# Optimization experiments

Measured on AMD Instinct MI355X. Metric: run time of the kernel, lower is better.

## Reference

```python
import jax, jax.numpy as jnp
import numpy as np

PATCH = 7
STRIDE = 1


def extract_patches(im, p=PATCH, stride=STRIDE):
    # im: [b, c, h, w] -> patches [b, N, c*p*p] (torch.nn.Unfold-style layout)
    pt = jax.lax.conv_general_dilated_patches(
        im, filter_shape=(p, p), window_strides=(stride, stride), padding='VALID')
    # pt: [b, c*p*p, h', w']
    b, d = pt.shape[0], pt.shape[1]
    return pt.reshape(b, d, -1).transpose(0, 2, 1)  # [b, N, d]


def coherence_swd(xp, yp, rand):
    # xp, yp: [N, d]; rand: [d, P]
    r = rand / jnp.std(rand, axis=0, keepdims=True, ddof=1)  # torch.std is unbiased
    px = xp @ r  # [N, P]
    py = yp @ r  # [N, P]
    ix = jnp.argsort(px, axis=0).T  # [P, N]
    iy = jnp.argsort(py, axis=0).T  # [P, N]
    # Gather full patch vectors by per-projection sorted order, L1 distance.
    # xp[ix]: [P, N, d] -- the big irregular-gather intermediate.
    diff = jnp.abs(xp[ix] - yp[iy])  # [P, N, d]
    # loss = (1/P) * sum_p mean(|...|_p); each term has identical size -> plain mean
    return diff.mean()


def setup_inputs() -> dict:
    key = jax.random.key(0)
    k1, k2, k3 = jax.random.split(key, 3)
    b, c, h, w = 1, 3, 96, 96
    d = c * PATCH * PATCH  # 147
    num_proj = 256
    x = jax.random.normal(k1, (b, c, h, w), dtype=jnp.float32)
    y = jax.random.normal(k2, (b, c, h, w), dtype=jnp.float32)
    rand = jax.random.normal(k3, (d, num_proj), dtype=jnp.float32)
    return {"x": x, "y": y, "rand": rand}


def reference(x, y, rand):
    x_patches = extract_patches(x)  # [b, N, d]
    y_patches = extract_patches(y)
    losses = jax.vmap(coherence_swd, in_axes=(0, 0, None))(x_patches, y_patches, rand)  # [b]
    return losses.mean()  # batch_reduction='mean'
```

## Files before the change

### kernel.cpp

```cpp
#include <hip/hip_runtime.h>

#define HH 96
#define WW 96
#define OH 90
#define OW 90
#define NPATCH 8100
#define DD 147
#define DPAD 148
#define NPROJ 256
#define TN 32
#define SORT_T 512
#define NBUCK 4096
#define KPT 16
#define PGRP 16
#define NCH 64
#define KPB2 128

typedef float vf2 __attribute__((ext_vector_type(2)));

__device__ __forceinline__ float l1_fp8x4(unsigned xw, unsigned yw, float acc) {
    const vf2 a0 = __builtin_amdgcn_cvt_pk_f32_fp8((int)xw, false);
    const vf2 a1 = __builtin_amdgcn_cvt_pk_f32_fp8((int)xw, true);
    const vf2 b0 = __builtin_amdgcn_cvt_pk_f32_fp8((int)yw, false);
    const vf2 b1 = __builtin_amdgcn_cvt_pk_f32_fp8((int)yw, true);
    acc += fabsf(a0.x - b0.x);
    acc += fabsf(a0.y - b0.y);
    acc += fabsf(a1.x - b1.x);
    acc += fabsf(a1.y - b1.y);
    return acc;
}

__global__ __launch_bounds__(512, 4)
void patch_proj_kernel(const float* __restrict__ x, const float* __restrict__ y,
                       const float* __restrict__ rnd,
                       int* __restrict__ xm8, int* __restrict__ ym8,
                       int* __restrict__ xt8, int* __restrict__ yt8,
                       float* __restrict__ pxT, float* __restrict__ pyT,
                       float* __restrict__ out)
{
    __shared__ float s[TN * DPAD];
    const int tid = threadIdx.x;
    const int n0 = blockIdx.x * TN;
    const int img = blockIdx.y;
    const float* __restrict__ src = img ? y : x;
    int* __restrict__ m8 = img ? ym8 : xm8;
    int* __restrict__ t8 = img ? yt8 : xt8;
    float* __restrict__ pT = img ? pyT : pxT;
    if (blockIdx.x == 0 && img == 0 && tid == 0) out[0] = 0.0f;

    for (int idx = tid; idx < TN * DPAD; idx += 512) {
        const int t = idx / DPAD;
        const int d = idx - t * DPAD;
        const int n = n0 + t;
        float v = 0.f;
        if (n < NPATCH && d < DD) {
            const int oy = n / OW, ox = n - oy * OW;
            const int c  = d / 49, r  = d - c * 49;
            const int di = r / 7,  dj = r - di * 7;
            v = src[c * (HH * WW) + (oy + di) * WW + (ox + dj)];
        }
        s[idx] = v;
    }
    __syncthreads();

    for (int idx = tid; idx < TN * 40; idx += 512) {
        const int t = idx / 40;
        const int u = idx - t * 40;
        const int n = n0 + t;
        if (n >= NPATCH) continue;
        int w = 0;
        if (u < 32) {
            const int d = 4 * u;
            w = __builtin_amdgcn_cvt_pk_fp8_f32(s[t*DPAD+d],   s[t*DPAD+d+1], w, false);
            w = __builtin_amdgcn_cvt_pk_fp8_f32(s[t*DPAD+d+2], s[t*DPAD+d+3], w, true);
            m8[(size_t)n * 32 + u] = w;
        } else {
            const int ut = u - 32;
            const int d = 128 + 4 * ut;
            const float v0 = (d     < DPAD) ? s[t*DPAD+d]     : 0.f;
            const float v1 = (d + 1 < DPAD) ? s[t*DPAD+d+1]   : 0.f;
            const float v2 = (d + 2 < DPAD) ? s[t*DPAD+d+2]   : 0.f;
            const float v3 = (d + 3 < DPAD) ? s[t*DPAD+d+3]   : 0.f;
            w = __builtin_amdgcn_cvt_pk_fp8_f32(v0, v1, w, false);
            w = __builtin_amdgcn_cvt_pk_fp8_f32(v2, v3, w, true);
            t8[(size_t)n * 8 + ut] = w;
        }
    }

    const int q2 = tid & 127;
    const int t0 = (tid >> 7) * 8;
    const float2* __restrict__ rnd2 = (const float2*)rnd;

    float acc[8][2];
#pragma unroll
    for (int t = 0; t < 8; ++t) { acc[t][0] = 0.f; acc[t][1] = 0.f; }

    for (int d = 0; d < 144; d += 4) {
        const float2 r0 = rnd2[(d + 0) * 128 + q2];
        const float2 r1 = rnd2[(d + 1) * 128 + q2];
        const float2 r2 = rnd2[(d + 2) * 128 + q2];
        const float2 r3 = rnd2[(d + 3) * 128 + q2];
#pragma unroll
        for (int t = 0; t < 8; ++t) {
            const float4 v = *(const float4*)&s[(t0 + t) * DPAD + d];
            acc[t][0] += v.x * r0.x + v.y * r1.x + v.z * r2.x + v.w * r3.x;
            acc[t][1] += v.x * r0.y + v.y * r1.y + v.z * r2.y + v.w * r3.y;
        }
    }
    {
        const float2 r0 = rnd2[144 * 128 + q2];
        const float2 r1 = rnd2[145 * 128 + q2];
        const float2 r2 = rnd2[146 * 128 + q2];
#pragma unroll
        for (int t = 0; t < 8; ++t) {
            const float4 v = *(const float4*)&s[(t0 + t) * DPAD + 144];
            acc[t][0] += v.x * r0.x + v.y * r1.x + v.z * r2.x;
            acc[t][1] += v.x * r0.y + v.y * r1.y + v.z * r2.y;
        }
    }

    const int nb = n0 + t0;
#pragma unroll
    for (int r = 0; r < 2; ++r) {
        float* row = pT + (size_t)(2 * q2 + r) * NPATCH + nb;
        if (nb + 7 < NPATCH) {
            float4 lo, hi;
            lo.x = acc[0][r]; lo.y = acc[1][r]; lo.z = acc[2][r]; lo.w = acc[3][r];
            hi.x = acc[4][r]; hi.y = acc[5][r]; hi.z = acc[6][r]; hi.w = acc[7][r];
            ((float4*)row)[0] = lo;
            ((float4*)row)[1] = hi;
        } else {
#pragma unroll
            for (int t = 0; t < 8; ++t)
                if (nb + t < NPATCH) row[t] = acc[t][r];
        }
    }
}

__global__ __launch_bounds__(SORT_T, 4)
void rank_kernel(const float* __restrict__ pT,
                 unsigned short* __restrict__ rxOut,
                 unsigned short* __restrict__ iyOut)
{
    __shared__ unsigned hist[NBUCK];
    __shared__ unsigned cnt[NBUCK];
    __shared__ float    skey[8192];
    __shared__ unsigned wsum[8];
    const int pb = blockIdx.x;
    const int tid = threadIdx.x;
    const int lane = tid & 63;
    const float* col = pT + (size_t)pb * NPATCH;

    {
        uint4 z = make_uint4(0, 0, 0, 0);
        ((uint4*)hist)[tid] = z;
        ((uint4*)hist)[tid + SORT_T] = z;
    }
    __syncthreads();

    float k[KPT];
    int bk[KPT];
#pragma unroll
    for (int t = 0; t < KPT; ++t) {
        const int i = tid + SORT_T * t;
        if (i < NPATCH) {
            const float v = col[i];
            k[t] = v;
            int b = (int)((v + 51.2f) * 40.0f);
            b = b < 0 ? 0 : (b > NBUCK - 1 ? NBUCK - 1 : b);
            bk[t] = b;
            atomicAdd(&hist[b], 1u);
        } else {
            k[t] = 0.f;
            bk[t] = -1;
        }
    }
    __syncthreads();

    {
        const int b0 = tid * 8;
        unsigned h[8];
#pragma unroll
        for (int q = 0; q < 8; ++q) h[q] = hist[b0 + q];
        unsigned tsum = 0;
#pragma unroll
        for (int q = 0; q < 8; ++q) tsum += h[q];
        unsigned acc = tsum;
#pragma unroll
        for (int d = 1; d < 64; d <<= 1) {
            const unsigned v = __shfl_up(acc, d, 64);
            if (lane >= d) acc += v;
        }
        const unsigned wexcl = acc - tsum;
        if (lane == 63) wsum[tid >> 6] = acc;
        __syncthreads();
        if (tid == 0) {
            unsigned roff = 0;
#pragma unroll
            for (int w = 0; w < 8; ++w) {
                const unsigned tt = wsum[w];
                wsum[w] = roff;
                roff += tt;
            }
        }
        __syncthreads();
        unsigned run = wsum[tid >> 6] + wexcl;
#pragma unroll
        for (int q = 0; q < 8; ++q) { cnt[b0 + q] = run; run += h[q]; }
    }
    __syncthreads();

#pragma unroll
    for (int t = 0; t < KPT; ++t) {
        if (bk[t] >= 0) {
            const unsigned pos = atomicAdd(&cnt[bk[t]], 1u);
            skey[pos] = k[t];
        }
    }
    __syncthreads();

#pragma unroll
    for (int t = 0; t < KPT; ++t) {
        const int i = tid + SORT_T * t;
        if (bk[t] < 0) continue;
        const int b = bk[t];
        const unsigned end = cnt[b];
        const unsigned cb = hist[b];
        const unsigned start = end - cb;
        const float myk = k[t];
        unsigned r = start;
        for (unsigned s2 = start; s2 < end; ++s2)
            r += (skey[s2] < myk) ? 1u : 0u;
        if (pb < NPROJ)
            rxOut[(size_t)pb * NPATCH + i] = (unsigned short)r;
        else
            iyOut[(size_t)(pb - NPROJ) * NPATCH + r] = (unsigned short)i;
    }
}

__global__ __launch_bounds__(256, 4)
void reduce_kernel(const uint4* __restrict__ xm8, const uint4* __restrict__ ym8,
                   const uint4* __restrict__ xt8, const uint4* __restrict__ yt8,
                   const unsigned short* __restrict__ rx,
                   const unsigned short* __restrict__ iy,
                   float* __restrict__ out)
{
    __shared__ unsigned short sp[PGRP * KPB2];
    const int p0 = blockIdx.y * PGRP;
    const int i0 = blockIdx.x * KPB2;
    const int iend = min(i0 + KPB2, NPATCH);
    const int tid = threadIdx.x;
    const int wave = tid >> 6, lane = tid & 63;

    for (int idx = tid; idx < PGRP * KPB2; idx += 256) {
        const int pp = idx >> 7, r = idx & 127;
        int src = i0 + r;
        src = src < NPATCH ? src : NPATCH - 1;
        const int p = p0 + pp;
        const unsigned short rk = rx[(size_t)p * NPATCH + src];
        const unsigned short j = iy[(size_t)p * NPATCH + rk];
        sp[idx] = j < NPATCH ? j : (unsigned short)(NPATCH - 1);
    }
    __syncthreads();

    float facc = 0.f;

    {
        const int g = lane >> 3;
        const int u = lane & 7;
#pragma unroll
        for (int it = 0; it < 4; ++it) {
            const int i = i0 + wave * 8 + it * 32;
            const uint4 xa = xm8[(size_t)i * 8 + lane];
            int jj[PGRP];
#pragma unroll
            for (int pp = 0; pp < PGRP; ++pp)
                jj[pp] = sp[pp * KPB2 + (i - i0) + g];
            uint4 ya[PGRP];
#pragma unroll
            for (int pp = 0; pp < PGRP; ++pp)
                ya[pp] = ym8[(size_t)jj[pp] * 8 + u];
            float tacc = 0.f;
#pragma unroll
            for (int pp = 0; pp < PGRP; ++pp) {
                tacc = l1_fp8x4(xa.x, ya[pp].x, tacc);
                tacc = l1_fp8x4(xa.y, ya[pp].y, tacc);
                tacc = l1_fp8x4(xa.z, ya[pp].z, tacc);
                tacc = l1_fp8x4(xa.w, ya[pp].w, tacc);
            }
            facc += (i + g < iend) ? tacc : 0.f;
        }
    }

    {
        const int g2 = lane >> 1;
        const int u2 = lane & 1;
        const int i2 = i0 + wave * 32;
        const uint4 xa = xt8[(size_t)i2 * 2 + lane];
        int jj[PGRP];
#pragma unroll
        for (int pp = 0; pp < PGRP; ++pp)
            jj[pp] = sp[pp * KPB2 + (i2 - i0) + g2];
        uint4 ya[PGRP];
#pragma unroll
        for (int pp = 0; pp < PGRP; ++pp)
            ya[pp] = yt8[(size_t)jj[pp] * 2 + u2];
        float tacc = 0.f;
#pragma unroll
        for (int pp = 0; pp < PGRP; ++pp) {
            tacc = l1_fp8x4(xa.x, ya[pp].x, tacc);
            tacc = l1_fp8x4(xa.y, ya[pp].y, tacc);
            tacc = l1_fp8x4(xa.z, ya[pp].z, tacc);
            tacc = l1_fp8x4(xa.w, ya[pp].w, tacc);
        }
        facc += (i2 + g2 < iend) ? tacc : 0.f;
    }

#pragma unroll
    for (int o = 32; o > 0; o >>= 1) facc += __shfl_down(facc, o, 64);

    __shared__ float sred[4];
    if (lane == 0) sred[wave] = facc;
    __syncthreads();
    if (tid == 0) {
        const float s = sred[0] + sred[1] + sred[2] + sred[3];
        atomicAdd(out, s * (1.0f / ((float)NPROJ * (float)NPATCH * (float)DD)));
    }
}

extern "C" void kernel_launch(void* const* d_in, const int* in_sizes, int n_in,
                              void* d_out, int out_size, void* d_ws, size_t ws_size,
                              hipStream_t stream)
{
    const float* x   = (const float*)d_in[0];
    const float* y   = (const float*)d_in[1];
    const float* rnd = (const float*)d_in[2];

    char* ws = (char*)d_ws;
    int* xm8 = (int*)(ws + 0);
    int* ym8 = (int*)(ws + 1036800);
    int* xt8 = (int*)(ws + 2073600);
    int* yt8 = (int*)(ws + 2332800);
    float* pxT = (float*)(ws + 2592000);
    float* pyT = (float*)(ws + 10886400);
    unsigned short* rx = (unsigned short*)(ws + 19180800);
    unsigned short* iy = (unsigned short*)(ws + 23328000);
    float* out = (float*)d_out;

    hipLaunchKernelGGL(patch_proj_kernel, dim3((NPATCH + TN - 1) / TN, 2), dim3(512), 0, stream,
                       x, y, rnd, xm8, ym8, xt8, yt8, pxT, pyT, out);
    hipLaunchKernelGGL(rank_kernel, dim3(2 * NPROJ), dim3(SORT_T), 0, stream,
                       pxT, rx, iy);
    hipLaunchKernelGGL(reduce_kernel, dim3(NCH, NPROJ / PGRP), dim3(256), 0, stream,
                       (const uint4*)xm8, (const uint4*)ym8,
                       (const uint4*)xt8, (const uint4*)yt8, rx, iy, out);
}
```

Before: 145.3 us.

## Compute patch projections with split-bf16 MFMA and hoist fp8 decode in reduce

Replaces the scalar FP32 patch-times-projection GEMM with bf16 MFMA 16x16x32. Each operand is split into hi/lo bf16 parts and three MFMAs are accumulated per tile to keep near-fp32 accuracy. A new prep kernel transposes and splits the random matrix, tile size doubles to 64 patches, and shared memory holds a fragment-ordered layout. In the reduce kernel, the x-side fp8 values are decoded once per row instead of per projection. The risks are an extra kernel launch and small precision differences that could change sort ranks.

Result: faster. 133.1 us (-8.4%).

```diff
diff --git a/kernel.cpp b/kernel.cpp
--- a/kernel.cpp
+++ b/kernel.cpp
@@ -6,9 +6,10 @@
 #define OW 90
 #define NPATCH 8100
 #define DD 147
-#define DPAD 148
 #define NPROJ 256
-#define TN 32
+#define TN 64
+#define KPAD 160
+#define NKS 5
 #define SORT_T 512
 #define NBUCK 4096
 #define KPT 16
@@ -17,28 +18,43 @@
 #define KPB2 128
 
 typedef float vf2 __attribute__((ext_vector_type(2)));
-
-__device__ __forceinline__ float l1_fp8x4(unsigned xw, unsigned yw, float acc) {
-    const vf2 a0 = __builtin_amdgcn_cvt_pk_f32_fp8((int)xw, false);
-    const vf2 a1 = __builtin_amdgcn_cvt_pk_f32_fp8((int)xw, true);
-    const vf2 b0 = __builtin_amdgcn_cvt_pk_f32_fp8((int)yw, false);
-    const vf2 b1 = __builtin_amdgcn_cvt_pk_f32_fp8((int)yw, true);
-    acc += fabsf(a0.x - b0.x);
-    acc += fabsf(a0.y - b0.y);
-    acc += fabsf(a1.x - b1.x);
-    acc += fabsf(a1.y - b1.y);
-    return acc;
+typedef short bf16x8 __attribute__((ext_vector_type(8)));
+typedef float f32x4 __attribute__((ext_vector_type(4)));
+
+__device__ __forceinline__ unsigned short bf16_rne(float f) {
+    unsigned u = __builtin_bit_cast(unsigned, f);
+    u += 0x7FFFu + ((u >> 16) & 1u);
+    return (unsigned short)(u >> 16);
+}
+__device__ __forceinline__ float bf16_f(unsigned short h) {
+    return __builtin_bit_cast(float, (unsigned)h << 16);
+}
+
+__global__ __launch_bounds__(1024)
+void prep_rnd_kernel(const float* __restrict__ rnd,
+                     unsigned short* __restrict__ rth,
+                     unsigned short* __restrict__ rtl)
+{
+    const int idx = blockIdx.x * 1024 + threadIdx.x;
+    const int k = idx >> 8;
+    const int p = idx & 255;
+    const float v = (k < DD) ? rnd[k * NPROJ + p] : 0.f;
+    const unsigned short hi = bf16_rne(v);
+    const unsigned short lo = bf16_rne(v - bf16_f(hi));
+    rth[p * KPAD + k] = hi;
+    rtl[p * KPAD + k] = lo;
 }
 
 __global__ __launch_bounds__(512, 4)
 void patch_proj_kernel(const float* __restrict__ x, const float* __restrict__ y,
-                       const float* __restrict__ rnd,
+                       const unsigned short* __restrict__ rth,
+                       const unsigned short* __restrict__ rtl,
                        int* __restrict__ xm8, int* __restrict__ ym8,
                        int* __restrict__ xt8, int* __restrict__ yt8,
                        float* __restrict__ pxT, float* __restrict__ pyT,
                        float* __restrict__ out)
 {
-    __shared__ float s[TN * DPAD];
+    __shared__ unsigned short sh[2][TN * KPAD];
     const int tid = threadIdx.x;
     const int n0 = blockIdx.x * TN;
     const int img = blockIdx.y;
@@ -48,9 +64,9 @@
     float* __restrict__ pT = img ? pyT : pxT;
     if (blockIdx.x == 0 && img == 0 && tid == 0) out[0] = 0.0f;
 
-    for (int idx = tid; idx < TN * DPAD; idx += 512) {
-        const int t = idx / DPAD;
-        const int d = idx - t * DPAD;
+    for (int idx = tid; idx < TN * KPAD; idx += 512) {
+        const int t = idx / KPAD;
+        const int d = idx - t * KPAD;
         const int n = n0 + t;
         float v = 0.f;
         if (n < NPATCH && d < DD) {
@@ -59,7 +75,13 @@
             const int di = r / 7,  dj = r - di * 7;
             v = src[c * (HH * WW) + (oy + di) * WW + (ox + dj)];
         }
-        s[idx] = v;
+        const unsigned short hi = bf16_rne(v);
+        const unsigned short lo = bf16_rne(v - bf16_f(hi));
+        const int mt = t >> 4, r16 = t & 15;
+        const int ks = d >> 5, q = (d & 31) >> 3, j = d & 7;
+        const int fidx = (((mt * NKS + ks) * 4 + q) * 16 + r16) * 8 + j;
+        sh[0][fidx] = hi;
+        sh[1][fidx] = lo;
     }
     __syncthreads();
 
@@ -68,71 +90,65 @@
         const int u = idx - t * 40;
         const int n = n0 + t;
         if (n >= NPATCH) continue;
+        const int d = 4 * u;
+        const int mt = t >> 4, r16 = t & 15;
+        const int ks = d >> 5, q = (d & 31) >> 3, jb = d & 7;
+        const ushort4 hv = *(const ushort4*)&sh[0][(((mt * NKS + ks) * 4 + q) * 16 + r16) * 8 + jb];
         int w = 0;
-        if (u < 32) {
-            const int d = 4 * u;
-            w = __builtin_amdgcn_cvt_pk_fp8_f32(s[t*DPAD+d],   s[t*DPAD+d+1], w, false);
-            w = __builtin_amdgcn_cvt_pk_fp8_f32(s[t*DPAD+d+2], s[t*DPAD+d+3], w, true);
-            m8[(size_t)n * 32 + u] = w;
-        } else {
-            const int ut = u - 32;
-            const int d = 128 + 4 * ut;
-            const float v0 = (d     < DPAD) ? s[t*DPAD+d]     : 0.f;
-            const float v1 = (d + 1 < DPAD) ? s[t*DPAD+d+1]   : 0.f;
-            const float v2 = (d + 2 < DPAD) ? s[t*DPAD+d+2]   : 0.f;
-            const float v3 = (d + 3 < DPAD) ? s[t*DPAD+d+3]   : 0.f;
-            w = __builtin_amdgcn_cvt_pk_fp8_f32(v0, v1, w, false);
-            w = __builtin_amdgcn_cvt_pk_fp8_f32(v2, v3, w, true);
-            t8[(size_t)n * 8 + ut] = w;
-        }
-    }
-
-    const int q2 = tid & 127;
-    const int t0 = (tid >> 7) * 8;
-    const float2* __restrict__ rnd2 = (const float2*)rnd;
-
-    float acc[8][2];
-#pragma unroll
-    for (int t = 0; t < 8; ++t) { acc[t][0] = 0.f; acc[t][1] = 0.f; }
-
-    for (int d = 0; d < 144; d += 4) {
-        const float2 r0 = rnd2[(d + 0) * 128 + q2];
-        const float2 r1 = rnd2[(d + 1) * 128 + q2];
-        const float2 r2 = rnd2[(d + 2) * 128 + q2];
-        const float2 r3 = rnd2[(d + 3) * 128 + q2];
-#pragma unroll
-        for (int t = 0; t < 8; ++t) {
-            const float4 v = *(const float4*)&s[(t0 + t) * DPAD + d];
-            acc[t][0] += v.x * r0.x + v.y * r1.x + v.z * r2.x + v.w * r3.x;
-            acc[t][1] += v.x * r0.y + v.y * r1.y + v.z * r2.y + v.w * r3.y;
-        }
-    }
-    {
-        const float2 r0 = rnd2[144 * 128 + q2];
-        const float2 r1 = rnd2[145 * 128 + q2];
-        const float2 r2 = rnd2[146 * 128 + q2];
-#pragma unroll
-        for (int t = 0; t < 8; ++t) {
-            const float4 v = *(const float4*)&s[(t0 + t) * DPAD + 144];
-            acc[t][0] += v.x * r0.x + v.y * r1.x + v.z * r2.x;
-            acc[t][1] += v.x * r0.y + v.y * r1.y + v.z * r2.y;
-        }
-    }
-
-    const int nb = n0 + t0;
-#pragma unroll
-    for (int r = 0; r < 2; ++r) {
-        float* row = pT + (size_t)(2 * q2 + r) * NPATCH + nb;
-        if (nb + 7 < NPATCH) {
-            float4 lo, hi;
-            lo.x = acc[0][r]; lo.y = acc[1][r]; lo.z = acc[2][r]; lo.w = acc[3][r];
-            hi.x = acc[4][r]; hi.y = acc[5][r]; hi.z = acc[6][r]; hi.w = acc[7][r];
-            ((float4*)row)[0] = lo;
-            ((float4*)row)[1] = hi;
-        } else {
-#pragma unroll
-            for (int t = 0; t < 8; ++t)
-                if (nb + t < NPATCH) row[t] = acc[t][r];
+        w = __builtin_amdgcn_cvt_pk_fp8_f32(bf16_f(hv.x), bf16_f(hv.y), w, false);
+        w = __builtin_amdgcn_cvt_pk_fp8_f32(bf16_f(hv.z), bf16_f(hv.w), w, true);
+        if (u < 32) m8[(size_t)n * 32 + u] = w;
+        else        t8[(size_t)n * 8 + (u - 32)] = w;
+    }
+
+    const int wv = tid >> 6, lane = tid & 63;
+    const int cl = lane & 15, qk = lane >> 4;
+
+    f32x4 acc[4][2];
+#pragma unroll
+    for (int mt = 0; mt < 4; ++mt)
+#pragma unroll
+        for (int nt = 0; nt < 2; ++nt)
+            acc[mt][nt] = (f32x4){0.f, 0.f, 0.f, 0.f};
+
+#pragma unroll
+    for (int ks = 0; ks < NKS; ++ks) {
+        const int ko = ks * 32 + qk * 8;
+        bf16x8 bh[2], bl[2];
+#pragma unroll
+        for (int nt = 0; nt < 2; ++nt) {
+            const int col = wv * 32 + nt * 16 + cl;
+            bh[nt] = *(const bf16x8*)&rth[col * KPAD + ko];
+            bl[nt] = *(const bf16x8*)&rtl[col * KPAD + ko];
+        }
+#pragma unroll
+        for (int mt = 0; mt < 4; ++mt) {
+            const int base = ((mt * NKS + ks) * 64 + lane) * 8;
+            const bf16x8 ah = *(const bf16x8*)&sh[0][base];
+            const bf16x8 al = *(const bf16x8*)&sh[1][base];
+#pragma unroll
+            for (int nt = 0; nt < 2; ++nt) {
+                acc[mt][nt] = __builtin_amdgcn_mfma_f32_16x16x32_bf16(ah, bh[nt], acc[mt][nt], 0, 0, 0);
+                acc[mt][nt] = __builtin_amdgcn_mfma_f32_16x16x32_bf16(ah, bl[nt], acc[mt][nt], 0, 0, 0);
+                acc[mt][nt] = __builtin_amdgcn_mfma_f32_16x16x32_bf16(al, bh[nt], acc[mt][nt], 0, 0, 0);
+            }
+        }
+    }
+
+#pragma unroll
+    for (int mt = 0; mt < 4; ++mt) {
+        const int patch = n0 + mt * 16 + qk * 4;
+#pragma unroll
+        for (int nt = 0; nt < 2; ++nt) {
+            const int proj = wv * 32 + nt * 16 + cl;
+            float* rowp = pT + (size_t)proj * NPATCH + patch;
+            if (patch + 3 < NPATCH) {
+                *(f32x4*)rowp = acc[mt][nt];
+            } else {
+#pragma unroll
+                for (int e = 0; e < 4; ++e)
+                    if (patch + e < NPATCH) rowp[e] = acc[mt][nt][e];
+            }
         }
     }
 }
@@ -238,6 +254,28 @@
     }
 }
 
+__device__ __forceinline__ void cvt16f(const uint4 w, float* o) {
+    vf2 t;
+    t = __builtin_amdgcn_cvt_pk_f32_fp8((int)w.x, false); o[0]  = t.x; o[1]  = t.y;
+    t = __builtin_amdgcn_cvt_pk_f32_fp8((int)w.x, true);  o[2]  = t.x; o[3]  = t.y;
+    t = __builtin_amdgcn_cvt_pk_f32_fp8((int)w.y, false); o[4]  = t.x; o[5]  = t.y;
+    t = __builtin_amdgcn_cvt_pk_f32_fp8((int)w.y, true);  o[6]  = t.x; o[7]  = t.y;
+    t = __builtin_amdgcn_cvt_pk_f32_fp8((int)w.z, false); o[8]  = t.x; o[9]  = t.y;
+    t = __builtin_amdgcn_cvt_pk_f32_fp8((int)w.z, true);  o[10] = t.x; o[11] = t.y;
+    t = __builtin_amdgcn_cvt_pk_f32_fp8((int)w.w, false); o[12] = t.x; o[13] = t.y;
+    t = __builtin_amdgcn_cvt_pk_f32_fp8((int)w.w, true);  o[14] = t.x; o[15] = t.y;
+}
+
+__device__ __forceinline__ float l1_vs4(const float* xf, unsigned yw, float acc) {
+    const vf2 b0 = __builtin_amdgcn_cvt_pk_f32_fp8((int)yw, false);
+    const vf2 b1 = __builtin_amdgcn_cvt_pk_f32_fp8((int)yw, true);
+    acc += fabsf(xf[0] - b0.x);
+    acc += fabsf(xf[1] - b0.y);
+    acc += fabsf(xf[2] - b1.x);
+    acc += fabsf(xf[3] - b1.y);
+    return acc;
+}
+
 __global__ __launch_bounds__(256, 4)
 void reduce_kernel(const uint4* __restrict__ xm8, const uint4* __restrict__ ym8,
                    const uint4* __restrict__ xt8, const uint4* __restrict__ yt8,
@@ -280,13 +318,15 @@
 #pragma unroll
             for (int pp = 0; pp < PGRP; ++pp)
                 ya[pp] = ym8[(size_t)jj[pp] * 8 + u];
+            float xf[16];
+            cvt16f(xa, xf);
             float tacc = 0.f;
 #pragma unroll
             for (int pp = 0; pp < PGRP; ++pp) {
-                tacc = l1_fp8x4(xa.x, ya[pp].x, tacc);
-                tacc = l1_fp8x4(xa.y, ya[pp].y, tacc);
-                tacc = l1_fp8x4(xa.z, ya[pp].z, tacc);
-                tacc = l1_fp8x4(xa.w, ya[pp].w, tacc);
+                tacc = l1_vs4(xf + 0,  ya[pp].x, tacc);
+                tacc = l1_vs4(xf + 4,  ya[pp].y, tacc);
+                tacc = l1_vs4(xf + 8,  ya[pp].z, tacc);
+                tacc = l1_vs4(xf + 12, ya[pp].w, tacc);
             }
             facc += (i + g < iend) ? tacc : 0.f;
         }
@@ -305,13 +345,15 @@
 #pragma unroll
         for (int pp = 0; pp < PGRP; ++pp)
             ya[pp] = yt8[(size_t)jj[pp] * 2 + u2];
+        float xf[16];
+        cvt16f(xa, xf);
         float tacc = 0.f;
 #pragma unroll
         for (int pp = 0; pp < PGRP; ++pp) {
-            tacc = l1_fp8x4(xa.x, ya[pp].x, tacc);
-            tacc = l1_fp8x4(xa.y, ya[pp].y, tacc);
-            tacc = l1_fp8x4(xa.z, ya[pp].z, tacc);
-            tacc = l1_fp8x4(xa.w, ya[pp].w, tacc);
+            tacc = l1_vs4(xf + 0,  ya[pp].x, tacc);
+            tacc = l1_vs4(xf + 4,  ya[pp].y, tacc);
+            tacc = l1_vs4(xf + 8,  ya[pp].z, tacc);
+            tacc = l1_vs4(xf + 12, ya[pp].w, tacc);
         }
         facc += (i2 + g2 < iend) ? tacc : 0.f;
     }
@@ -345,10 +387,14 @@
     float* pyT = (float*)(ws + 10886400);
     unsigned short* rx = (unsigned short*)(ws + 19180800);
     unsigned short* iy = (unsigned short*)(ws + 23328000);
+    unsigned short* rth = (unsigned short*)(ws + 27475200);
+    unsigned short* rtl = (unsigned short*)(ws + 27557120);
     float* out = (float*)d_out;
 
+    hipLaunchKernelGGL(prep_rnd_kernel, dim3(40), dim3(1024), 0, stream,
+                       rnd, rth, rtl);
     hipLaunchKernelGGL(patch_proj_kernel, dim3((NPATCH + TN - 1) / TN, 2), dim3(512), 0, stream,
-                       x, y, rnd, xm8, ym8, xt8, yt8, pxT, pyT, out);
+                       x, y, rth, rtl, xm8, ym8, xt8, yt8, pxT, pyT, out);
     hipLaunchKernelGGL(rank_kernel, dim3(2 * NPROJ), dim3(SORT_T), 0, stream,
                        pxT, rx, iy);
     hipLaunchKernelGGL(reduce_kernel, dim3(NCH, NPROJ / PGRP), dim3(256), 0, stream,
```
